# Kernel tuning notes

Measured on AMD Instinct MI355X. Metric: run time of the kernel, lower is better.

The kernel has to match this reference:

```python
import jax, jax.numpy as jnp
import numpy as np

B, GS, IN_H, GCN_H, LIN_H = 65536, 7, 5, 144, 128


def _xavier(key, shape):
    fan_in, fan_out = shape[0], shape[1]
    limit = np.sqrt(6.0 / (fan_in + fan_out)).astype(np.float32)
    return jax.random.uniform(key, shape, jnp.float32, -limit, limit)


def setup_inputs() -> dict:
    key = jax.random.key(0)
    ks = jax.random.split(key, 12)
    operations = jax.random.normal(ks[0], (B, GS, IN_H), jnp.float32)
    adjacency = (jax.random.uniform(ks[1], (B, GS, GS)) < 0.3).astype(jnp.float32)
    num_vertices = jax.random.randint(ks[2], (B,), 1, 8).astype(jnp.float32)
    w1_0 = _xavier(ks[3], (IN_H, GCN_H))
    w2_0 = _xavier(ks[4], (IN_H, GCN_H))
    w1_1 = _xavier(ks[5], (GCN_H, GCN_H))
    w2_1 = _xavier(ks[6], (GCN_H, GCN_H))
    w1_2 = _xavier(ks[7], (GCN_H, GCN_H))
    w2_2 = _xavier(ks[8], (GCN_H, GCN_H))
    fc1_w = _xavier(ks[9], (LIN_H, GCN_H))  # torch Linear stores [out, in]
    fc2_w = _xavier(ks[10], (1, LIN_H))
    return {
        'operations': operations, 'adjacency': adjacency, 'num_vertices': num_vertices,
        'w1_0': w1_0, 'w2_0': w2_0, 'w1_1': w1_1, 'w2_1': w2_1,
        'w1_2': w1_2, 'w2_2': w2_2, 'fc1_w': fc1_w, 'fc2_w': fc2_w,
    }


def _row_normalize(adj):
    # divide each row by its sum (matches torch normalize_adj)
    return adj / adj.sum(axis=2, keepdims=True)


def reference(operations, adjacency, num_vertices,
              w1_0, w2_0, w1_1, w2_1, w1_2, w2_2, fc1_w, fc2_w):
    gs = adjacency.shape[1]
    eye = jnp.eye(gs, dtype=adjacency.dtype)
    adj_d = _row_normalize(adjacency + eye)  # [B, gs, gs]
    x = operations
    for w1, w2 in ((w1_0, w2_0), (w1_1, w2_1), (w1_2, w2_2)):
        norm_adj = _row_normalize(adj_d)                      # identity in value, kept faithful
        inv_norm_adj = _row_normalize(adj_d.transpose(0, 2, 1))
        o1 = jax.nn.relu(jnp.einsum('bij,bjk->bik', norm_adj, x @ w1))
        o2 = jax.nn.relu(jnp.einsum('bij,bjk->bik', inv_norm_adj, x @ w2))
        x = (o1 + o2) * 0.5  # dropout is identity at inference
    pooled = x.sum(axis=1) / num_vertices[:, None]            # [B, gcn_hidden]
    h = pooled @ fc1_w.T                                      # [B, linear_hidden]
    out = (h @ fc2_w.T).reshape(-1)                           # [B]
    return out
```

## Files before the change

### kernel.cpp

```cpp
#include <hip/hip_runtime.h>


typedef _Float16 half8   __attribute__((ext_vector_type(8)));
typedef _Float16 half4_t __attribute__((ext_vector_type(4)));
typedef float    floatx16 __attribute__((ext_vector_type(16)));

constexpr int GS = 7;
constexpr int NI = 8;
constexpr int MROWS = NI * GS;
constexpr int H = 144;
constexpr int LSTRIDE = 2 * 5 * 9 * 512;
constexpr int WT_HALFS = 3 * LSTRIDE;
constexpr int FRAGS = 3 * 90 * 64;

static __device__ inline half8 bc(_Float16 v) {
    half8 h = {v, v, v, v, v, v, v, v};
    return h;
}

__global__ void prep_kernel(const float* __restrict__ w10, const float* __restrict__ w20,
                            const float* __restrict__ w11, const float* __restrict__ w21,
                            const float* __restrict__ w12, const float* __restrict__ w22,
                            const float* __restrict__ fc1, const float* __restrict__ fc2,
                            _Float16* __restrict__ wt, float* __restrict__ g)
{
    if (blockIdx.x == 68) {
        const int j = threadIdx.x;
        if (j < H) {
            float s = 0.f;
            for (int o = 0; o < 128; ++o) s = fmaf(fc2[o], fc1[o * H + j], s);
            g[j] = s;
        }
        return;
    }
    const int t = blockIdx.x * 256 + threadIdx.x;
    if (t >= FRAGS) return;
    const int l    = t / (90 * 64);
    const int r    = t - l * (90 * 64);
    const int frag = r >> 6;
    const int lane = r & 63;
    const int p    = frag / 45;
    const int rem  = frag - p * 45;
    const int nt   = rem / 9;
    const int ks   = rem - nt * 9;
    const int n    = nt * 32 + (lane & 31);
    const int k0   = ks * 16 + (lane >> 5) * 8;
    const float* W = (l == 0) ? (p ? w20 : w10)
                   : (l == 1) ? (p ? w21 : w11)
                              : (p ? w22 : w12);
    const int K = (l == 0) ? 5 : 144;
    half8 h = bc((_Float16)0);
    #pragma unroll
    for (int j = 0; j < 8; ++j) {
        const int k = k0 + j;
        if (n < H && k < K) h[j] = (_Float16)W[k * H + n];
    }
    *(half8*)(wt + (size_t)l * LSTRIDE + (size_t)frag * 512 + (size_t)lane * 8) = h;
}

template<int NK, int CB>
static __device__ __forceinline__ void layer_pass(const _Float16* __restrict__ wl,
                                                  const int tid, const int lane, const int wv,
                                                  _Float16 (*sX)[152],
                                                  _Float16 (*sXn)[152], _Float16 (*sXi)[152],
                                                  const _Float16 (*sAh)[2][GS][8])
{
    for (int u = tid; u < MROWS * CB; u += 256) {
        const int row = u / CB, cb = u - row * CB;
        const int item = row / GS, rr = row - item * GS;
        const int c0 = cb * 8;
        const half8 aN = *(const half8*)&sAh[item][0][rr][0];
        const half8 aI = *(const half8*)&sAh[item][1][rr][0];
        half8 an = bc((_Float16)0), ai = bc((_Float16)0);
        #pragma unroll
        for (int j = 0; j < GS; ++j) {
            const half8 xj = *(const half8*)&sX[item * GS + j][c0];
            an += bc(aN[j]) * xj;
            ai += bc(aI[j]) * xj;
        }
        *(half8*)&sXn[row][c0] = an;
        *(half8*)&sXi[row][c0] = ai;
    }
    __syncthreads();

    const int  nt    = wv;
    const bool extra = (wv >= 2);
    const int  em    = wv & 1;
    const int  khi   = (lane >> 5) * 8;
    const int  r0    = lane & 31;
    const int  r1    = 32 + r0;
    const int  r1c   = (r1 < MROWS) ? r1 : (MROWS - 1);

    floatx16 a1m0, a1m1, a2m0, a2m1, e1, e2;
    #pragma unroll
    for (int i = 0; i < 16; ++i) {
        a1m0[i] = 0.f; a1m1[i] = 0.f; a2m0[i] = 0.f; a2m1[i] = 0.f;
        e1[i] = 0.f; e2[i] = 0.f;
    }

    #pragma unroll
    for (int ks = 0; ks < NK; ++ks) {
        const int c = ks * 16 + khi;
        const half8 bn0 = *(const half8*)&sXn[r0][c];
        const half8 bn1 = *(const half8*)&sXn[r1c][c];
        const half8 bi0 = *(const half8*)&sXi[r0][c];
        const half8 bi1 = *(const half8*)&sXi[r1c][c];
        const _Float16* f1 = wl + (size_t)((nt * 9 + ks) * 512) + (size_t)lane * 8;
        const half8 A1 = *(const half8*)f1;
        const half8 A2 = *(const half8*)(f1 + 45 * 512);
        a1m0 = __builtin_amdgcn_mfma_f32_32x32x16_f16(A1, bn0, a1m0, 0, 0, 0);
        a1m1 = __builtin_amdgcn_mfma_f32_32x32x16_f16(A1, bn1, a1m1, 0, 0, 0);
        a2m0 = __builtin_amdgcn_mfma_f32_32x32x16_f16(A2, bi0, a2m0, 0, 0, 0);
        a2m1 = __builtin_amdgcn_mfma_f32_32x32x16_f16(A2, bi1, a2m1, 0, 0, 0);
        if (extra) {
            const _Float16* f4 = wl + (size_t)((36 + ks) * 512) + (size_t)lane * 8;
            const half8 E1 = *(const half8*)f4;
            const half8 E2 = *(const half8*)(f4 + 45 * 512);
            e1 = __builtin_amdgcn_mfma_f32_32x32x16_f16(E1, em ? bn1 : bn0, e1, 0, 0, 0);
            e2 = __builtin_amdgcn_mfma_f32_32x32x16_f16(E2, em ? bi1 : bi0, e2, 0, 0, 0);
        }
    }

    #pragma unroll
    for (int q = 0; q < 4; ++q) {
        const int n0 = nt * 32 + 4 * (lane >> 5) + 8 * q;
        half4_t h0, h1;
        #pragma unroll
        for (int i = 0; i < 4; ++i) {
            float v1 = a1m0[4 * q + i]; v1 = v1 > 0.f ? v1 : 0.f;
            float v2 = a2m0[4 * q + i]; v2 = v2 > 0.f ? v2 : 0.f;
            h0[i] = (_Float16)(0.5f * (v1 + v2));
            float w1 = a1m1[4 * q + i]; w1 = w1 > 0.f ? w1 : 0.f;
            float w2 = a2m1[4 * q + i]; w2 = w2 > 0.f ? w2 : 0.f;
            h1[i] = (_Float16)(0.5f * (w1 + w2));
        }
        *(half4_t*)&sX[r0][n0] = h0;
        if (r0 < MROWS - 32) *(half4_t*)&sX[r1][n0] = h1;
    }
    if (extra) {
        #pragma unroll
        for (int q = 0; q < 2; ++q) {
            const int n0 = 128 + 4 * (lane >> 5) + 8 * q;
            half4_t h;
            #pragma unroll
            for (int i = 0; i < 4; ++i) {
                float v1 = e1[4 * q + i]; v1 = v1 > 0.f ? v1 : 0.f;
                float v2 = e2[4 * q + i]; v2 = v2 > 0.f ? v2 : 0.f;
                h[i] = (_Float16)(0.5f * (v1 + v2));
            }
            const int rr = em * 32 + r0;
            if (rr < MROWS) *(half4_t*)&sX[rr][n0] = h;
        }
    }
    __syncthreads();
}

__global__ __launch_bounds__(256, 3)
void gcn_mfma(const float* __restrict__ ops, const float* __restrict__ adj,
              const float* __restrict__ nv,
              const _Float16* __restrict__ wt, const float* __restrict__ gw,
              float* __restrict__ out)
{
    __shared__ __align__(16) _Float16 sX [MROWS][152];
    __shared__ __align__(16) _Float16 sXn[MROWS][152];
    __shared__ __align__(16) _Float16 sXi[MROWS][152];
    __shared__ __align__(16) _Float16 sAh[NI][2][GS][8];

    float (*adjd)[GS][GS] = (float(*)[GS][GS])&sXn[0][0];

    const int tid  = threadIdx.x;
    const int lane = tid & 63;
    const int wv   = tid >> 6;
    const int ibase = blockIdx.x * NI;

    if (tid < MROWS) {
        const int item = tid / GS, r = tid % GS;
        const float* orow = ops + ((size_t)(ibase + item) * GS + r) * 5;
        half8 h = bc((_Float16)0);
        h[0] = (_Float16)orow[0]; h[1] = (_Float16)orow[1]; h[2] = (_Float16)orow[2];
        h[3] = (_Float16)orow[3]; h[4] = (_Float16)orow[4];
        *(half8*)&sX[tid][0] = h;
        *(half8*)&sX[tid][8] = bc((_Float16)0);

        const float* arow = adj + ((size_t)(ibase + item) * GS + r) * GS;
        float a[GS]; float sm = 0.f;
        #pragma unroll
        for (int c = 0; c < GS; ++c) { a[c] = arow[c] + (c == r ? 1.f : 0.f); sm += a[c]; }
        const float is = 1.f / sm;
        #pragma unroll
        for (int c = 0; c < GS; ++c) {
            const float v = a[c] * is;
            adjd[item][r][c] = v;
            sAh[item][0][r][c] = (_Float16)v;
        }
        sAh[item][0][r][7] = (_Float16)0.f;
    }
    __syncthreads();
    if (tid < MROWS) {
        const int item = tid / GS, r = tid % GS;
        float v[GS]; float sm = 0.f;
        #pragma unroll
        for (int k = 0; k < GS; ++k) { v[k] = adjd[item][k][r]; sm += v[k]; }
        const float is = 1.f / sm;
        #pragma unroll
        for (int k = 0; k < GS; ++k) sAh[item][1][r][k] = (_Float16)(v[k] * is);
        sAh[item][1][r][7] = (_Float16)0.f;
    }
    __syncthreads();

    layer_pass<1, 2>(wt,                        tid, lane, wv, sX, sXn, sXi, sAh);
    layer_pass<9, 18>(wt + (size_t)1 * LSTRIDE, tid, lane, wv, sX, sXn, sXi, sAh);
    layer_pass<9, 18>(wt + (size_t)2 * LSTRIDE, tid, lane, wv, sX, sXn, sXi, sAh);

    if (tid < NI * 16) {
        const int item = tid >> 4, part = tid & 15;
        float s = 0.f;
        #pragma unroll
        for (int c = 0; c < 9; ++c) {
            const int j = part * 9 + c;
            const float gj = gw[j];
            #pragma unroll
            for (int i = 0; i < GS; ++i)
                s = fmaf((float)sX[item * GS + i][j], gj, s);
        }
        s += __shfl_xor(s, 1);
        s += __shfl_xor(s, 2);
        s += __shfl_xor(s, 4);
        s += __shfl_xor(s, 8);
        if (part == 0) out[ibase + item] = s / nv[ibase + item];
    }
}

extern "C" void kernel_launch(void* const* d_in, const int* in_sizes, int n_in,
                              void* d_out, int out_size, void* d_ws, size_t ws_size,
                              hipStream_t stream) {
    const float* ops = (const float*)d_in[0];
    const float* adj = (const float*)d_in[1];
    const float* nv  = (const float*)d_in[2];
    const float* w10 = (const float*)d_in[3];
    const float* w20 = (const float*)d_in[4];
    const float* w11 = (const float*)d_in[5];
    const float* w21 = (const float*)d_in[6];
    const float* w12 = (const float*)d_in[7];
    const float* w22 = (const float*)d_in[8];
    const float* fc1 = (const float*)d_in[9];
    const float* fc2 = (const float*)d_in[10];

    _Float16* wt = (_Float16*)d_ws;
    float*    g  = (float*)((char*)d_ws + (size_t)WT_HALFS * 2);

    prep_kernel<<<69, 256, 0, stream>>>(w10, w20, w11, w21, w12, w22,
                                        fc1, fc2, wt, g);
    gcn_mfma<<<65536 / NI, 256, 0, stream>>>(ops, adj, nv, wt, g, (float*)d_out);
}
```

Before: 271.3 us.

## Halve items per block and compute the ragged column tile with 16x16x32 MFMA

Each block now handles 4 graphs (28 rows) instead of 8, so each wave does one 32-row M tile instead of two. The leftover 16 output columns (128..143) are computed with 16x16x32 MFMA tiles split across two waves instead of a 32-wide tile that was mostly padding. The weight prep layout is changed to match, and launch bounds are raised to allow more resident blocks. This cuts wasted MFMA work and shared memory per block to raise occupancy. In exchange it doubles the number of blocks and redundant weight fragment loads per graph, and adds zero-padding of shared buffers.

```diff
diff --git a/kernel.cpp b/kernel.cpp
--- a/kernel.cpp
+++ b/kernel.cpp
@@ -4,14 +4,18 @@
 typedef _Float16 half8   __attribute__((ext_vector_type(8)));
 typedef _Float16 half4_t __attribute__((ext_vector_type(4)));
 typedef float    floatx16 __attribute__((ext_vector_type(16)));
+typedef float    floatx4  __attribute__((ext_vector_type(4)));
 
 constexpr int GS = 7;
-constexpr int NI = 8;
+constexpr int NI = 4;
 constexpr int MROWS = NI * GS;
 constexpr int H = 144;
-constexpr int LSTRIDE = 2 * 5 * 9 * 512;
+constexpr int T4OFF   = 2 * 4 * 9 * 512;
+constexpr int LSTRIDE = T4OFF + 2 * 5 * 512;
 constexpr int WT_HALFS = 3 * LSTRIDE;
-constexpr int FRAGS = 3 * 90 * 64;
+constexpr int MAIN_T = 3 * 2 * 4 * 9 * 64;
+constexpr int T4_T   = 3 * 2 * 5 * 64;
+constexpr int XROW   = 152;
 
 static __device__ inline half8 bc(_Float16 v) {
     half8 h = {v, v, v, v, v, v, v, v};
@@ -24,7 +28,7 @@
                             const float* __restrict__ fc1, const float* __restrict__ fc2,
                             _Float16* __restrict__ wt, float* __restrict__ g)
 {
-    if (blockIdx.x == 68) {
+    if (blockIdx.x == 62) {
         const int j = threadIdx.x;
         if (j < H) {
             float s = 0.f;
@@ -34,35 +38,60 @@
         return;
     }
     const int t = blockIdx.x * 256 + threadIdx.x;
-    if (t >= FRAGS) return;
-    const int l    = t / (90 * 64);
-    const int r    = t - l * (90 * 64);
-    const int frag = r >> 6;
-    const int lane = r & 63;
-    const int p    = frag / 45;
-    const int rem  = frag - p * 45;
-    const int nt   = rem / 9;
-    const int ks   = rem - nt * 9;
-    const int n    = nt * 32 + (lane & 31);
-    const int k0   = ks * 16 + (lane >> 5) * 8;
-    const float* W = (l == 0) ? (p ? w20 : w10)
-                   : (l == 1) ? (p ? w21 : w11)
-                              : (p ? w22 : w12);
-    const int K = (l == 0) ? 5 : 144;
-    half8 h = bc((_Float16)0);
-    #pragma unroll
-    for (int j = 0; j < 8; ++j) {
-        const int k = k0 + j;
-        if (n < H && k < K) h[j] = (_Float16)W[k * H + n];
-    }
-    *(half8*)(wt + (size_t)l * LSTRIDE + (size_t)frag * 512 + (size_t)lane * 8) = h;
+    if (t < MAIN_T) {
+        const int l    = t / 4608;
+        const int r    = t - l * 4608;
+        const int frag = r >> 6;
+        const int lane = r & 63;
+        const int p    = frag / 36;
+        const int rem  = frag - p * 36;
+        const int nt   = rem / 9;
+        const int ks   = rem - nt * 9;
+        const int n    = nt * 32 + (lane & 31);
+        const int k0   = ks * 16 + (lane >> 5) * 8;
+        const float* W = (l == 0) ? (p ? w20 : w10)
+                       : (l == 1) ? (p ? w21 : w11)
+                                  : (p ? w22 : w12);
+        const int K = (l == 0) ? 5 : H;
+        half8 h = bc((_Float16)0);
+        #pragma unroll
+        for (int j = 0; j < 8; ++j) {
+            const int k = k0 + j;
+            if (k < K) h[j] = (_Float16)W[k * H + n];
+        }
+        *(half8*)(wt + (size_t)l * LSTRIDE + (size_t)((p * 4 + nt) * 9 + ks) * 512
+                     + (size_t)lane * 8) = h;
+    } else {
+        const int t2 = t - MAIN_T;
+        if (t2 >= T4_T) return;
+        const int l    = t2 / 640;
+        const int r    = t2 - l * 640;
+        const int frag = r >> 6;
+        const int lane = r & 63;
+        const int p    = frag / 5;
+        const int ks   = frag - p * 5;
+        const int n    = 128 + (lane & 15);
+        const int k0   = ks * 32 + (lane >> 4) * 8;
+        const float* W = (l == 0) ? (p ? w20 : w10)
+                       : (l == 1) ? (p ? w21 : w11)
+                                  : (p ? w22 : w12);
+        const int K = (l == 0) ? 5 : H;
+        half8 h = bc((_Float16)0);
+        #pragma unroll
+        for (int j = 0; j < 8; ++j) {
+            const int k = k0 + j;
+            if (k < K) h[j] = (_Float16)W[k * H + n];
+        }
+        *(half8*)(wt + (size_t)l * LSTRIDE + T4OFF + (size_t)(p * 5 + ks) * 512
+                     + (size_t)lane * 8) = h;
+    }
 }
 
 template<int NK, int CB>
 static __device__ __forceinline__ void layer_pass(const _Float16* __restrict__ wl,
                                                   const int tid, const int lane, const int wv,
-                                                  _Float16 (*sX)[152],
-                                                  _Float16 (*sXn)[152], _Float16 (*sXi)[152],
+                                                  _Float16 (*sX)[XROW],
+                                                  _Float16 (*sXn)[XROW], _Float16 (*sXi)[XROW],
                                                   const _Float16 (*sAh)[2][GS][8])
 {
     for (int u = tid; u < MROWS * CB; u += 256) {
@@ -85,86 +114,83 @@
 
     const int  nt    = wv;
     const bool extra = (wv >= 2);
-    const int  em    = wv & 1;
+    const int  mt    = wv & 1;
     const int  khi   = (lane >> 5) * 8;
     const int  r0    = lane & 31;
-    const int  r1    = 32 + r0;
-    const int  r1c   = (r1 < MROWS) ? r1 : (MROWS - 1);
-
-    floatx16 a1m0, a1m1, a2m0, a2m1, e1, e2;
+    const int  r0c   = (r0 < MROWS) ? r0 : (MROWS - 1);
+    const int  rr4r  = mt * 16 + (lane & 15);
+    const int  rr4   = (rr4r < MROWS) ? rr4r : (MROWS - 1);
+
+    floatx16 a1, a2;
+    floatx4  e1, e2;
     #pragma unroll
-    for (int i = 0; i < 16; ++i) {
-        a1m0[i] = 0.f; a1m1[i] = 0.f; a2m0[i] = 0.f; a2m1[i] = 0.f;
-        e1[i] = 0.f; e2[i] = 0.f;
-    }
+    for (int i = 0; i < 16; ++i) { a1[i] = 0.f; a2[i] = 0.f; }
+    #pragma unroll
+    for (int i = 0; i < 4; ++i)  { e1[i] = 0.f; e2[i] = 0.f; }
 
     #pragma unroll
     for (int ks = 0; ks < NK; ++ks) {
         const int c = ks * 16 + khi;
-        const half8 bn0 = *(const half8*)&sXn[r0][c];
-        const half8 bn1 = *(const half8*)&sXn[r1c][c];
-        const half8 bi0 = *(const half8*)&sXi[r0][c];
-        const half8 bi1 = *(const half8*)&sXi[r1c][c];
+        const half8 bn = *(const half8*)&sXn[r0c][c];
+        const half8 bi = *(const half8*)&sXi[r0c][c];
         const _Float16* f1 = wl + (size_t)((nt * 9 + ks) * 512) + (size_t)lane * 8;
         const half8 A1 = *(const half8*)f1;
-        const half8 A2 = *(const half8*)(f1 + 45 * 512);
-        a1m0 = __builtin_amdgcn_mfma_f32_32x32x16_f16(A1, bn0, a1m0, 0, 0, 0);
-        a1m1 = __builtin_amdgcn_mfma_f32_32x32x16_f16(A1, bn1, a1m1, 0, 0, 0);
-        a2m0 = __builtin_amdgcn_mfma_f32_32x32x16_f16(A2, bi0, a2m0, 0, 0, 0);
-        a2m1 = __builtin_amdgcn_mfma_f32_32x32x16_f16(A2, bi1, a2m1, 0, 0, 0);
-        if (extra) {
-            const _Float16* f4 = wl + (size_t)((36 + ks) * 512) + (size_t)lane * 8;
+        const half8 A2 = *(const half8*)(f1 + 36 * 512);
+        a1 = __builtin_amdgcn_mfma_f32_32x32x16_f16(A1, bn, a1, 0, 0, 0);
+        a2 = __builtin_amdgcn_mfma_f32_32x32x16_f16(A2, bi, a2, 0, 0, 0);
+        if (extra && !(ks & 1)) {
+            const int t4 = ks >> 1;
+            const int k4 = t4 * 32 + (lane >> 4) * 8;
+            const half8 b4n = *(const half8*)&sXn[rr4][k4];
+            const half8 b4i = *(const half8*)&sXi[rr4][k4];
+            const _Float16* f4 = wl + T4OFF + (size_t)(t4 * 512) + (size_t)lane * 8;
             const half8 E1 = *(const half8*)f4;
-            const half8 E2 = *(const half8*)(f4 + 45 * 512);
-            e1 = __builtin_amdgcn_mfma_f32_32x32x16_f16(E1, em ? bn1 : bn0, e1, 0, 0, 0);
-            e2 = __builtin_amdgcn_mfma_f32_32x32x16_f16(E2, em ? bi1 : bi0, e2, 0, 0, 0);
-        }
-    }
-
-    #pragma unroll
-    for (int q = 0; q < 4; ++q) {
-        const int n0 = nt * 32 + 4 * (lane >> 5) + 8 * q;
-        half4_t h0, h1;
-        #pragma unroll
-        for (int i = 0; i < 4; ++i) {
-            float v1 = a1m0[4 * q + i]; v1 = v1 > 0.f ? v1 : 0.f;
-            float v2 = a2m0[4 * q + i]; v2 = v2 > 0.f ? v2 : 0.f;
-            h0[i] = (_Float16)(0.5f * (v1 + v2));
-            float w1 = a1m1[4 * q + i]; w1 = w1 > 0.f ? w1 : 0.f;
-            float w2 = a2m1[4 * q + i]; w2 = w2 > 0.f ? w2 : 0.f;
-            h1[i] = (_Float16)(0.5f * (w1 + w2));
-        }
-        *(half4_t*)&sX[r0][n0] = h0;
-        if (r0 < MROWS - 32) *(half4_t*)&sX[r1][n0] = h1;
-    }
-    if (extra) {
-        #pragma unroll
-        for (int q = 0; q < 2; ++q) {
-            const int n0 = 128 + 4 * (lane >> 5) + 8 * q;
-            half4_t h;
+            const half8 E2 = *(const half8*)(f4 + 5 * 512);
+            e1 = __builtin_amdgcn_mfma_f32_16x16x32_f16(E1, b4n, e1, 0, 0, 0);
+            e2 = __builtin_amdgcn_mfma_f32_16x16x32_f16(E2, b4i, e2, 0, 0, 0);
+        }
+    }
+
+    if (r0 < MROWS) {
+        #pragma unroll
+        for (int q = 0; q < 4; ++q) {
+            const int n0 = nt * 32 + 4 * (lane >> 5) + 8 * q;
+            half4_t h0;
             #pragma unroll
             for (int i = 0; i < 4; ++i) {
-                float v1 = e1[4 * q + i]; v1 = v1 > 0.f ? v1 : 0.f;
-                float v2 = e2[4 * q + i]; v2 = v2 > 0.f ? v2 : 0.f;
-                h[i] = (_Float16)(0.5f * (v1 + v2));
+                float v1 = a1[4 * q + i]; v1 = v1 > 0.f ? v1 : 0.f;
+                float v2 = a2[4 * q + i]; v2 = v2 > 0.f ? v2 : 0.f;
+                h0[i] = (_Float16)(0.5f * (v1 + v2));
             }
-            const int rr = em * 32 + r0;
-            if (rr < MROWS) *(half4_t*)&sX[rr][n0] = h;
-        }
-    }
-    __syncthreads();
-}
-
-__global__ __launch_bounds__(256, 3)
+            *(half4_t*)&sX[r0][n0] = h0;
+        }
+    }
+    if (extra && rr4r < MROWS) {
+        const int n0 = 128 + (lane >> 4) * 4;
+        half4_t h;
+        #pragma unroll
+        for (int i = 0; i < 4; ++i) {
+            float v1 = e1[i]; v1 = v1 > 0.f ? v1 : 0.f;
+            float v2 = e2[i]; v2 = v2 > 0.f ? v2 : 0.f;
+            h[i] = (_Float16)(0.5f * (v1 + v2));
+        }
+        *(half4_t*)&sX[rr4r][n0] = h;
+    }
+    __syncthreads();
+}
+
+__global__ __launch_bounds__(256, 5)
 void gcn_mfma(const float* __restrict__ ops, const float* __restrict__ adj,
               const float* __restrict__ nv,
               const _Float16* __restrict__ wt, const float* __restrict__ gw,
               float* __restrict__ out)
 {
-    __shared__ __align__(16) _Float16 sX [MROWS][152];
-    __shared__ __align__(16) _Float16 sXn[MROWS][152];
-    __shared__ __align__(16) _Float16 sXi[MROWS][152];
+    __shared__ __align__(16) _Float16 sMem[3 * MROWS * XROW + 16];
     __shared__ __align__(16) _Float16 sAh[NI][2][GS][8];
+
+    _Float16 (*sX)[XROW]  = (_Float16(*)[XROW])&sMem[0];
+    _Float16 (*sXn)[XROW] = (_Float16(*)[XROW])&sMem[MROWS * XROW];
+    _Float16 (*sXi)[XROW] = (_Float16(*)[XROW])&sMem[2 * MROWS * XROW];
 
     float (*adjd)[GS][GS] = (float(*)[GS][GS])&sXn[0][0];
 
@@ -207,6 +233,19 @@
         sAh[item][1][r][7] = (_Float16)0.f;
     }
     __syncthreads();
+
+    if (tid < MROWS) {
+        const half8 z = bc((_Float16)0);
+        *(half8*)&sXn[tid][16]  = z; *(half8*)&sXn[tid][24]  = z;
+        *(half8*)&sXi[tid][16]  = z; *(half8*)&sXi[tid][24]  = z;
+        *(half8*)&sXn[tid][144] = z;
+        *(half8*)&sXi[tid][144] = z;
+    }
+    if (tid == 32) {
+        const half8 z = bc((_Float16)0);
+        *(half8*)&sMem[3 * MROWS * XROW]     = z;
+        *(half8*)&sMem[3 * MROWS * XROW + 8] = z;
+    }
 
     layer_pass<1, 2>(wt,                        tid, lane, wv, sX, sXn, sXi, sAh);
     layer_pass<9, 18>(wt + (size_t)1 * LSTRIDE, tid, lane, wv, sX, sXn, sXi, sAh);
@@ -249,7 +288,7 @@
     _Float16* wt = (_Float16*)d_ws;
     float*    g  = (float*)((char*)d_ws + (size_t)WT_HALFS * 2);
 
-    prep_kernel<<<69, 256, 0, stream>>>(w10, w20, w11, w21, w12, w22,
+    prep_kernel<<<63, 256, 0, stream>>>(w10, w20, w11, w21, w12, w22,
                                         fc1, fc2, wt, g);
     gcn_mfma<<<65536 / NI, 256, 0, stream>>>(ops, adj, nv, wt, g, (float*)d_out);
 }
```

New measurement: 263.1 us. 1.03x faster.

## Reorder GCN layer to X@W first, then block-diagonal adjacency MFMA

Applied to the files above, without the earlier changes.

Each layer now computes X@W1 and X@W2 with MFMA first, stages the results transposed in LDS, and applies the normalized and inverse adjacency as block-diagonal 32x32 MFMA fragments held in registers. This replaces the earlier VALU adjacency pre-multiply and the two large intermediate LDS buffers. Items per block drop from 8 to 4 so the 28 rows fit one MFMA tile, and launch bounds rise to 5 blocks per CU. In exchange, wave 0 handles the fifth column tile alone, which unbalances the waves, and each block fetches the same weight fragments over twice as many blocks.

```diff
diff --git a/kernel.cpp b/kernel.cpp
--- a/kernel.cpp
+++ b/kernel.cpp
@@ -6,12 +6,14 @@
 typedef float    floatx16 __attribute__((ext_vector_type(16)));
 
 constexpr int GS = 7;
-constexpr int NI = 8;
+constexpr int NI = 4;
 constexpr int MROWS = NI * GS;
 constexpr int H = 144;
 constexpr int LSTRIDE = 2 * 5 * 9 * 512;
 constexpr int WT_HALFS = 3 * LSTRIDE;
 constexpr int FRAGS = 3 * 90 * 64;
+constexpr int XROW = 152;
+constexpr int YROW = 40;
 
 static __device__ inline half8 bc(_Float16 v) {
     half8 h = {v, v, v, v, v, v, v, v};
@@ -43,134 +45,122 @@
     const int rem  = frag - p * 45;
     const int nt   = rem / 9;
     const int ks   = rem - nt * 9;
-    const int n    = nt * 32 + (lane & 31);
+    const int m    = nt * 32 + (lane & 31);
     const int k0   = ks * 16 + (lane >> 5) * 8;
     const float* W = (l == 0) ? (p ? w20 : w10)
                    : (l == 1) ? (p ? w21 : w11)
                               : (p ? w22 : w12);
-    const int K = (l == 0) ? 5 : 144;
+    const int K = (l == 0) ? 5 : H;
     half8 h = bc((_Float16)0);
     #pragma unroll
     for (int j = 0; j < 8; ++j) {
         const int k = k0 + j;
-        if (n < H && k < K) h[j] = (_Float16)W[k * H + n];
+        if (m < H && k < K) h[j] = (_Float16)W[k * H + m];
     }
     *(half8*)(wt + (size_t)l * LSTRIDE + (size_t)frag * 512 + (size_t)lane * 8) = h;
 }
 
-template<int NK, int CB>
+template<int NK>
 static __device__ __forceinline__ void layer_pass(const _Float16* __restrict__ wl,
-                                                  const int tid, const int lane, const int wv,
-                                                  _Float16 (*sX)[152],
-                                                  _Float16 (*sXn)[152], _Float16 (*sXi)[152],
-                                                  const _Float16 (*sAh)[2][GS][8])
+        const int lane, const int wv, const int hi, const int m32, const int r0c,
+        _Float16 (*sX)[XROW], _Float16 (*sYT)[32][YROW],
+        const half8 fN0, const half8 fN1, const half8 fI0, const half8 fI1)
 {
-    for (int u = tid; u < MROWS * CB; u += 256) {
-        const int row = u / CB, cb = u - row * CB;
-        const int item = row / GS, rr = row - item * GS;
-        const int c0 = cb * 8;
-        const half8 aN = *(const half8*)&sAh[item][0][rr][0];
-        const half8 aI = *(const half8*)&sAh[item][1][rr][0];
-        half8 an = bc((_Float16)0), ai = bc((_Float16)0);
-        #pragma unroll
-        for (int j = 0; j < GS; ++j) {
-            const half8 xj = *(const half8*)&sX[item * GS + j][c0];
-            an += bc(aN[j]) * xj;
-            ai += bc(aI[j]) * xj;
-        }
-        *(half8*)&sXn[row][c0] = an;
-        *(half8*)&sXi[row][c0] = ai;
-    }
-    __syncthreads();
-
-    const int  nt    = wv;
-    const bool extra = (wv >= 2);
-    const int  em    = wv & 1;
-    const int  khi   = (lane >> 5) * 8;
-    const int  r0    = lane & 31;
-    const int  r1    = 32 + r0;
-    const int  r1c   = (r1 < MROWS) ? r1 : (MROWS - 1);
-
-    floatx16 a1m0, a1m1, a2m0, a2m1, e1, e2;
-    #pragma unroll
-    for (int i = 0; i < 16; ++i) {
-        a1m0[i] = 0.f; a1m1[i] = 0.f; a2m0[i] = 0.f; a2m1[i] = 0.f;
-        e1[i] = 0.f; e2[i] = 0.f;
-    }
-
-    #pragma unroll
-    for (int ks = 0; ks < NK; ++ks) {
-        const int c = ks * 16 + khi;
-        const half8 bn0 = *(const half8*)&sXn[r0][c];
-        const half8 bn1 = *(const half8*)&sXn[r1c][c];
-        const half8 bi0 = *(const half8*)&sXi[r0][c];
-        const half8 bi1 = *(const half8*)&sXi[r1c][c];
-        const _Float16* f1 = wl + (size_t)((nt * 9 + ks) * 512) + (size_t)lane * 8;
-        const half8 A1 = *(const half8*)f1;
-        const half8 A2 = *(const half8*)(f1 + 45 * 512);
-        a1m0 = __builtin_amdgcn_mfma_f32_32x32x16_f16(A1, bn0, a1m0, 0, 0, 0);
-        a1m1 = __builtin_amdgcn_mfma_f32_32x32x16_f16(A1, bn1, a1m1, 0, 0, 0);
-        a2m0 = __builtin_amdgcn_mfma_f32_32x32x16_f16(A2, bi0, a2m0, 0, 0, 0);
-        a2m1 = __builtin_amdgcn_mfma_f32_32x32x16_f16(A2, bi1, a2m1, 0, 0, 0);
-        if (extra) {
-            const _Float16* f4 = wl + (size_t)((36 + ks) * 512) + (size_t)lane * 8;
-            const half8 E1 = *(const half8*)f4;
-            const half8 E2 = *(const half8*)(f4 + 45 * 512);
-            e1 = __builtin_amdgcn_mfma_f32_32x32x16_f16(E1, em ? bn1 : bn0, e1, 0, 0, 0);
-            e2 = __builtin_amdgcn_mfma_f32_32x32x16_f16(E2, em ? bi1 : bi0, e2, 0, 0, 0);
-        }
-    }
-
-    #pragma unroll
-    for (int q = 0; q < 4; ++q) {
-        const int n0 = nt * 32 + 4 * (lane >> 5) + 8 * q;
-        half4_t h0, h1;
-        #pragma unroll
-        for (int i = 0; i < 4; ++i) {
-            float v1 = a1m0[4 * q + i]; v1 = v1 > 0.f ? v1 : 0.f;
-            float v2 = a2m0[4 * q + i]; v2 = v2 > 0.f ? v2 : 0.f;
-            h0[i] = (_Float16)(0.5f * (v1 + v2));
-            float w1 = a1m1[4 * q + i]; w1 = w1 > 0.f ? w1 : 0.f;
-            float w2 = a2m1[4 * q + i]; w2 = w2 > 0.f ? w2 : 0.f;
-            h1[i] = (_Float16)(0.5f * (w1 + w2));
-        }
-        *(half4_t*)&sX[r0][n0] = h0;
-        if (r0 < MROWS - 32) *(half4_t*)&sX[r1][n0] = h1;
-    }
-    if (extra) {
-        #pragma unroll
-        for (int q = 0; q < 2; ++q) {
-            const int n0 = 128 + 4 * (lane >> 5) + 8 * q;
+    floatx16 m1a, m1b;
+
+    auto phaseA = [&](int t, floatx16& m1) {
+        floatx16 a1, a2;
+        #pragma unroll
+        for (int i = 0; i < 16; ++i) { a1[i] = 0.f; a2[i] = 0.f; }
+        #pragma unroll
+        for (int ks = 0; ks < NK; ++ks) {
+            const half8 xa = *(const half8*)&sX[r0c][ks * 16 + hi * 8];
+            const _Float16* fb = wl + (size_t)((t * 9 + ks) * 512) + (size_t)lane * 8;
+            const half8 B1 = *(const half8*)fb;
+            const half8 B2 = *(const half8*)(fb + 45 * 512);
+            a1 = __builtin_amdgcn_mfma_f32_32x32x16_f16(xa, B1, a1, 0, 0, 0);
+            a2 = __builtin_amdgcn_mfma_f32_32x32x16_f16(xa, B2, a2, 0, 0, 0);
+        }
+        #pragma unroll
+        for (int q = 0; q < 4; ++q) {
+            const int n0 = 8 * q + 4 * hi;
             half4_t h;
             #pragma unroll
-            for (int i = 0; i < 4; ++i) {
-                float v1 = e1[4 * q + i]; v1 = v1 > 0.f ? v1 : 0.f;
-                float v2 = e2[4 * q + i]; v2 = v2 > 0.f ? v2 : 0.f;
-                h[i] = (_Float16)(0.5f * (v1 + v2));
+            for (int i = 0; i < 4; ++i) h[i] = (_Float16)a1[4 * q + i];
+            *(half4_t*)&sYT[t][m32][n0] = h;
+        }
+        #pragma unroll
+        for (int i = 0; i < 16; ++i) m1[i] = 0.f;
+        {
+            const half8 y0 = *(const half8*)&sYT[t][m32][hi * 8];
+            m1 = __builtin_amdgcn_mfma_f32_32x32x16_f16(fN0, y0, m1, 0, 0, 0);
+            const half8 y1 = *(const half8*)&sYT[t][m32][16 + hi * 8];
+            m1 = __builtin_amdgcn_mfma_f32_32x32x16_f16(fN1, y1, m1, 0, 0, 0);
+        }
+        #pragma unroll
+        for (int q = 0; q < 4; ++q) {
+            const int n0 = 8 * q + 4 * hi;
+            half4_t h;
+            #pragma unroll
+            for (int i = 0; i < 4; ++i) h[i] = (_Float16)a2[4 * q + i];
+            *(half4_t*)&sYT[t][m32][n0] = h;
+        }
+    };
+
+    phaseA(wv, m1a);
+    if (wv == 0) phaseA(4, m1b);
+
+    __syncthreads();
+
+    auto phaseB = [&](int t, const floatx16& m1, int colbase, bool colok) {
+        floatx16 m2;
+        #pragma unroll
+        for (int i = 0; i < 16; ++i) m2[i] = 0.f;
+        const half8 y0 = *(const half8*)&sYT[t][m32][hi * 8];
+        m2 = __builtin_amdgcn_mfma_f32_32x32x16_f16(fI0, y0, m2, 0, 0, 0);
+        const half8 y1 = *(const half8*)&sYT[t][m32][16 + hi * 8];
+        m2 = __builtin_amdgcn_mfma_f32_32x32x16_f16(fI1, y1, m2, 0, 0, 0);
+        if (colok) {
+            const int col = colbase + m32;
+            #pragma unroll
+            for (int q = 0; q < 4; ++q) {
+                if (q < 3 || hi == 0) {
+                    #pragma unroll
+                    for (int i = 0; i < 4; ++i) {
+                        const int n = i + 8 * q + 4 * hi;
+                        float v1 = m1[4 * q + i]; v1 = v1 > 0.f ? v1 : 0.f;
+                        float v2 = m2[4 * q + i]; v2 = v2 > 0.f ? v2 : 0.f;
+                        sX[n][col] = (_Float16)(0.5f * (v1 + v2));
+                    }
+                }
             }
-            const int rr = em * 32 + r0;
-            if (rr < MROWS) *(half4_t*)&sX[rr][n0] = h;
-        }
-    }
-    __syncthreads();
-}
-
-__global__ __launch_bounds__(256, 3)
+        }
+    };
+
+    phaseB(wv, m1a, wv * 32, true);
+    if (wv == 0) phaseB(4, m1b, 128, m32 < 16);
+
+    __syncthreads();
+}
+
+__global__ __launch_bounds__(256, 5)
 void gcn_mfma(const float* __restrict__ ops, const float* __restrict__ adj,
               const float* __restrict__ nv,
               const _Float16* __restrict__ wt, const float* __restrict__ gw,
               float* __restrict__ out)
 {
-    __shared__ __align__(16) _Float16 sX [MROWS][152];
-    __shared__ __align__(16) _Float16 sXn[MROWS][152];
-    __shared__ __align__(16) _Float16 sXi[MROWS][152];
+    __shared__ __align__(16) _Float16 sX[MROWS][XROW];
+    __shared__ __align__(16) _Float16 sYT[5][32][YROW];
     __shared__ __align__(16) _Float16 sAh[NI][2][GS][8];
 
-    float (*adjd)[GS][GS] = (float(*)[GS][GS])&sXn[0][0];
+    float (*adjd)[GS][GS] = (float(*)[GS][GS])&sYT[0][0][0];
 
     const int tid  = threadIdx.x;
     const int lane = tid & 63;
     const int wv   = tid >> 6;
+    const int hi   = lane >> 5;
+    const int m32  = lane & 31;
+    const int r0c  = (m32 < MROWS) ? m32 : (MROWS - 1);
     const int ibase = blockIdx.x * NI;
 
     if (tid < MROWS) {
@@ -208,9 +198,31 @@
     }
     __syncthreads();
 
-    layer_pass<1, 2>(wt,                        tid, lane, wv, sX, sXn, sXi, sAh);
-    layer_pass<9, 18>(wt + (size_t)1 * LSTRIDE, tid, lane, wv, sX, sXn, sXi, sAh);
-    layer_pass<9, 18>(wt + (size_t)2 * LSTRIDE, tid, lane, wv, sX, sXn, sXi, sAh);
+    half8 fN0, fN1, fI0, fI1;
+    {
+        const int gA = m32 / 7;
+        const int rA = m32 - gA * 7;
+        #pragma unroll
+        for (int s = 0; s < 2; ++s) {
+            half8 fn = bc((_Float16)0), fi = bc((_Float16)0);
+            #pragma unroll
+            for (int j = 0; j < 8; ++j) {
+                const int k  = s * 16 + hi * 8 + j;
+                const int gK = k / 7;
+                const int rK = k - gK * 7;
+                if (m32 < MROWS && k < MROWS && gK == gA) {
+                    fn[j] = sAh[gA][0][rA][rK];
+                    fi[j] = sAh[gA][1][rA][rK];
+                }
+            }
+            if (s == 0) { fN0 = fn; fI0 = fi; }
+            else        { fN1 = fn; fI1 = fi; }
+        }
+    }
+
+    layer_pass<1>(wt,                        lane, wv, hi, m32, r0c, sX, sYT, fN0, fN1, fI0, fI1);
+    layer_pass<9>(wt + (size_t)1 * LSTRIDE,  lane, wv, hi, m32, r0c, sX, sYT, fN0, fN1, fI0, fI1);
+    layer_pass<9>(wt + (size_t)2 * LSTRIDE,  lane, wv, hi, m32, r0c, sX, sYT, fN0, fN1, fI0, fI1);
 
     if (tid < NI * 16) {
         const int item = tid >> 4, part = tid & 15;
```

New measurement: 501.7 us. 85.0% more time.
